# Kernel optimization log

Measured on AMD Instinct MI355X. Metric: run time of the kernel, lower is better.

The kernel has to match this reference:

```python
import jax, jax.numpy as jnp
import numpy as np

N_NODES = 100000
N_EDGES = 1600000
D_IN = 64
D_OUT = 64
BN_EPS = 1e-5


def setup_inputs() -> dict:
    key = jax.random.key(0)
    k1, k2, k3 = jax.random.split(key, 3)
    x = jax.random.normal(k1, (N_NODES, D_IN), dtype=jnp.float32)
    edge_index = jax.random.randint(k2, (2, N_EDGES), 0, N_NODES, dtype=jnp.int64)
    # GCNConv linear weight [out, in], glorot-ish scale
    W = jax.random.normal(k3, (D_OUT, D_IN), dtype=jnp.float32) / np.sqrt(D_IN)
    b = jnp.zeros((D_OUT,), dtype=jnp.float32)
    gamma = jnp.ones((D_OUT,), dtype=jnp.float32)
    beta = jnp.zeros((D_OUT,), dtype=jnp.float32)
    return {"x": x, "edge_index": edge_index, "W": W, "b": b, "gamma": gamma, "beta": beta}


def reference(x, edge_index, W, b, gamma, beta):
    # --- GCNConv: h = x @ W^T, propagate with sym-normalized adjacency + self-loops ---
    h = x @ W.T  # [N, D_OUT]
    src, tgt = edge_index[0], edge_index[1]
    # degree at target nodes, +1 for self-loop
    deg = jax.ops.segment_sum(jnp.ones((src.shape[0],), h.dtype), tgt,
                              num_segments=N_NODES) + 1.0  # [N]
    dinv = jax.lax.rsqrt(deg)
    norm = dinv[src] * dinv[tgt]  # [E]
    # gather -> scale -> scatter-add; self-loop contribution is h / deg
    agg = jax.ops.segment_sum(h[src] * norm[:, None], tgt, num_segments=N_NODES)
    out = agg + h * (1.0 / deg)[:, None] + b  # [N, D_OUT]
    # --- BatchNorm1d (training-mode batch statistics, biased variance) ---
    mean = out.mean(axis=0)
    var = out.var(axis=0)
    y = gamma * (out - mean) * jax.lax.rsqrt(var + BN_EPS) + beta
    # --- ReLU (dropout = identity in eval) ---
    return jax.nn.relu(y)
```

## Files before the change

kernel.cpp:

```cpp
#include <hip/hip_runtime.h>
#include <stdint.h>

#define N_NODES_C 100000
#define N_EDGES_C 1600000
#define DIM 64
#define BN_EPS_C 1e-5f
#define BSH 7
#define NB 782
#define CH 8192

__device__ __forceinline__ int ld_idx(const void* p, int is64, size_t i) {
    if (is64) return (int)((const long long*)p)[i];
    return ((const int*)p)[i];
}

__device__ __forceinline__ float bflo(unsigned int u) {
    return __uint_as_float(u << 16);
}
__device__ __forceinline__ float bfhi(unsigned int u) {
    return __uint_as_float(u & 0xFFFF0000u);
}
__device__ __forceinline__ unsigned short f2bf(float f) {
    unsigned int u = __float_as_uint(f);
    return (unsigned short)((u + 0x7FFF + ((u >> 16) & 1)) >> 16);
}

__global__ void probe_kernel(const unsigned int* __restrict__ p, int* __restrict__ flag) {
    if (threadIdx.x == 0 && blockIdx.x == 0) {
        int is64 = 1;
        for (int i = 1; i < 64; i += 2) {
            if (p[i] != 0u) { is64 = 0; break; }
        }
        *flag = is64;
    }
}

__global__ __launch_bounds__(256) void hist_kernel(const void* __restrict__ ei,
                                                   const int* __restrict__ flag,
                                                   int* __restrict__ bucket_cnt) {
    __shared__ int hist[NB];
    for (int i = threadIdx.x; i < NB; i += 256) hist[i] = 0;
    __syncthreads();
    int is64 = *flag;
    int stride = gridDim.x * blockDim.x;
    for (int e = blockIdx.x * blockDim.x + threadIdx.x; e < N_EDGES_C; e += stride) {
        int tg = ld_idx(ei, is64, (size_t)N_EDGES_C + e);
        atomicAdd(&hist[tg >> BSH], 1);
    }
    __syncthreads();
    for (int i = threadIdx.x; i < NB; i += 256) {
        int c = hist[i];
        if (c) atomicAdd(&bucket_cnt[i], c);
    }
}

__global__ __launch_bounds__(1024) void bucketscan_kernel(const int* __restrict__ bucket_cnt,
                                                          int* __restrict__ bucket_base,
                                                          int* __restrict__ bucket_cursor) {
    __shared__ int s[1024];
    int t = threadIdx.x;
    int v = (t < NB) ? bucket_cnt[t] : 0;
    s[t] = v;
    __syncthreads();
    for (int off = 1; off < 1024; off <<= 1) {
        int u = (t >= off) ? s[t - off] : 0;
        __syncthreads();
        s[t] += u;
        __syncthreads();
    }
    if (t < NB) {
        int excl = s[t] - v;
        bucket_base[t] = excl;
        bucket_cursor[t] = excl;
    }
}

__global__ __launch_bounds__(256) void binscatter_kernel(const void* __restrict__ ei,
                                                         const int* __restrict__ flag,
                                                         int* __restrict__ bucket_cursor,
                                                         unsigned int* __restrict__ csr) {
    __shared__ int hist[NB];
    __shared__ int base[NB];
    int is64 = *flag;
    int e0 = blockIdx.x * CH;
    int eend = min(e0 + CH, N_EDGES_C);
    for (int i = threadIdx.x; i < NB; i += 256) hist[i] = 0;
    __syncthreads();
    for (int e = e0 + threadIdx.x; e < eend; e += 256) {
        int tg = ld_idx(ei, is64, (size_t)N_EDGES_C + e);
        atomicAdd(&hist[tg >> BSH], 1);
    }
    __syncthreads();
    for (int i = threadIdx.x; i < NB; i += 256) {
        int c = hist[i];
        base[i] = c ? atomicAdd(&bucket_cursor[i], c) : 0;
        hist[i] = 0;
    }
    __syncthreads();
    for (int e = e0 + threadIdx.x; e < eend; e += 256) {
        int s  = ld_idx(ei, is64, (size_t)e);
        int tg = ld_idx(ei, is64, (size_t)N_EDGES_C + e);
        int b  = tg >> BSH;
        int tl = tg & 127;
        int pos = base[b] + atomicAdd(&hist[b], 1);
        csr[pos] = ((unsigned int)tl << 17) | (unsigned int)s;
    }
}

__global__ __launch_bounds__(256) void sort_kernel(const unsigned int* __restrict__ csr,
                                                   const int* __restrict__ bucket_base,
                                                   const int* __restrict__ bucket_cnt,
                                                   int* __restrict__ csr2,
                                                   int* __restrict__ rowbase,
                                                   float* __restrict__ dinv,
                                                   float* __restrict__ inv) {
    __shared__ int cnt[128];
    __shared__ int sbase[129];
    __shared__ int cur[128];
    int bk = blockIdx.x;
    int t = threadIdx.x;
    if (t < 128) cnt[t] = 0;
    __syncthreads();
    int base = bucket_base[bk], n = bucket_cnt[bk];
    for (int i = t; i < n; i += 256) {
        atomicAdd(&cnt[csr[base + i] >> 17], 1);
    }
    __syncthreads();
    if (t == 0) {
        int run = 0;
        for (int k = 0; k < 128; ++k) { sbase[k] = run; run += cnt[k]; }
        sbase[128] = run;
    }
    __syncthreads();
    if (t < 128) {
        cur[t] = base + sbase[t];
        int node = (bk << BSH) + t;
        if (node < N_NODES_C) {
            rowbase[node] = base + sbase[t];
            float d = (float)(cnt[t] + 1);
            dinv[node] = rsqrtf(d);
            inv[node]  = 1.0f / d;
        }
    }
    if (bk == 0 && t == 0) rowbase[N_NODES_C] = N_EDGES_C;
    __syncthreads();
    for (int i = t; i < n; i += 256) {
        unsigned int v = csr[base + i];
        int tl = v >> 17;
        int pos = atomicAdd(&cur[tl], 1);
        csr2[pos] = (int)(v & 0x1FFFF);
    }
}

__global__ __launch_bounds__(256) void gemm_kernel(const float* __restrict__ x,
                                                   const float* __restrict__ W,
                                                   unsigned short* __restrict__ hb) {
    __shared__ float Wl[DIM * 65];
    __shared__ float xs[32][DIM];
    int t = threadIdx.x;
    for (int i = t; i < DIM * DIM; i += 256) {
        Wl[(i >> 6) * 65 + (i & 63)] = W[i];
    }
    int r0 = blockIdx.x * 32;
    for (int i = t; i < 32 * DIM; i += 256) {
        int row = i >> 6, col = i & 63;
        int r = r0 + row;
        xs[row][col] = (r < N_NODES_C) ? x[(size_t)r * DIM + col] : 0.0f;
    }
    __syncthreads();
    int wv = t >> 6, c = t & 63;
    for (int it = 0; it < 8; ++it) {
        int rl = it * 4 + wv;
        int r = r0 + rl;
        float acc = 0.0f;
#pragma unroll
        for (int k = 0; k < DIM; ++k) acc += xs[rl][k] * Wl[c * 65 + k];
        if (r < N_NODES_C) hb[(size_t)r * DIM + c] = f2bf(acc);
    }
}

__global__ __launch_bounds__(256) void gather_kernel(const int* __restrict__ csr2,
                                                     const int* __restrict__ rowbase,
                                                     const float* __restrict__ dinv,
                                                     const float* __restrict__ inv,
                                                     const unsigned int* __restrict__ h2,
                                                     const float* __restrict__ b_,
                                                     float2* __restrict__ out,
                                                     float* __restrict__ sums,
                                                     float* __restrict__ sumsq) {
    int lane = threadIdx.x & 63;
    int half = lane >> 5;
    int c2 = lane & 31;
    int wid = blockIdx.x * (blockDim.x >> 6) + (threadIdx.x >> 6);
    int nw = gridDim.x * (blockDim.x >> 6);
    float2 bb = ((const float2*)b_)[c2];
    float s0a = 0.0f, q0a = 0.0f, s1a = 0.0f, q1a = 0.0f;
    for (int p = wid; p < N_NODES_C / 2; p += nw) {
        int t = 2 * p + half;
        int base = rowbase[t];
        int n = rowbase[t + 1] - base;
        float dt = dinv[t];
        float a0 = 0.0f, a1 = 0.0f;
        int j = 0;
        for (; j + 4 <= n; j += 4) {
            int sA = csr2[base + j + 0];
            int sB = csr2[base + j + 1];
            int sC = csr2[base + j + 2];
            int sD = csr2[base + j + 3];
            float wA = dinv[sA] * dt;
            float wB = dinv[sB] * dt;
            float wC = dinv[sC] * dt;
            float wD = dinv[sD] * dt;
            unsigned int uA = h2[(size_t)sA * 32 + c2];
            unsigned int uB = h2[(size_t)sB * 32 + c2];
            unsigned int uC = h2[(size_t)sC * 32 + c2];
            unsigned int uD = h2[(size_t)sD * 32 + c2];
            a0 = fmaf(bflo(uA), wA, a0); a1 = fmaf(bfhi(uA), wA, a1);
            a0 = fmaf(bflo(uB), wB, a0); a1 = fmaf(bfhi(uB), wB, a1);
            a0 = fmaf(bflo(uC), wC, a0); a1 = fmaf(bfhi(uC), wC, a1);
            a0 = fmaf(bflo(uD), wD, a0); a1 = fmaf(bfhi(uD), wD, a1);
        }
        for (; j < n; ++j) {
            int s = csr2[base + j];
            float w = dinv[s] * dt;
            unsigned int u = h2[(size_t)s * 32 + c2];
            a0 = fmaf(bflo(u), w, a0);
            a1 = fmaf(bfhi(u), w, a1);
        }
        unsigned int ut = h2[(size_t)t * 32 + c2];
        float it = inv[t];
        a0 = fmaf(bflo(ut), it, a0) + bb.x;
        a1 = fmaf(bfhi(ut), it, a1) + bb.y;
        out[(size_t)t * 32 + c2] = make_float2(a0, a1);
        s0a += a0; q0a += a0 * a0;
        s1a += a1; q1a += a1 * a1;
    }
    __shared__ float r0[256], r1[256], r2[256], r3[256];
    r0[threadIdx.x] = s0a; r1[threadIdx.x] = q0a;
    r2[threadIdx.x] = s1a; r3[threadIdx.x] = q1a;
    __syncthreads();
    if (threadIdx.x < 32) {
        float S0 = 0, Q0 = 0, S1 = 0, Q1 = 0;
        for (int k = threadIdx.x; k < 256; k += 32) {
            S0 += r0[k]; Q0 += r1[k]; S1 += r2[k]; Q1 += r3[k];
        }
        unsafeAtomicAdd(&sums[2 * threadIdx.x], S0);
        unsafeAtomicAdd(&sums[2 * threadIdx.x + 1], S1);
        unsafeAtomicAdd(&sumsq[2 * threadIdx.x], Q0);
        unsafeAtomicAdd(&sumsq[2 * threadIdx.x + 1], Q1);
    }
}

__global__ void bnparam_kernel(const float* __restrict__ sums,
                               const float* __restrict__ sumsq,
                               const float* __restrict__ gamma,
                               const float* __restrict__ beta,
                               float* __restrict__ scale,
                               float* __restrict__ shift) {
    int c = threadIdx.x;
    if (c < DIM) {
        float m = sums[c] * (1.0f / N_NODES_C);
        float var = sumsq[c] * (1.0f / N_NODES_C) - m * m;
        float sc = gamma[c] * rsqrtf(var + BN_EPS_C);
        scale[c] = sc;
        shift[c] = beta[c] - m * sc;
    }
}

__global__ __launch_bounds__(256) void bnrelu_kernel(float4* __restrict__ out,
                                                     const float* __restrict__ scale,
                                                     const float* __restrict__ shift) {
    const int n4 = N_NODES_C * (DIM / 4);
    int stride = gridDim.x * blockDim.x;
    for (int i = blockIdx.x * blockDim.x + threadIdx.x; i < n4; i += stride) {
        int cb = (i & 15) * 4;
        float4 v = out[i];
        v.x = fmaxf(fmaf(v.x, scale[cb + 0], shift[cb + 0]), 0.0f);
        v.y = fmaxf(fmaf(v.y, scale[cb + 1], shift[cb + 1]), 0.0f);
        v.z = fmaxf(fmaf(v.z, scale[cb + 2], shift[cb + 2]), 0.0f);
        v.w = fmaxf(fmaf(v.w, scale[cb + 3], shift[cb + 3]), 0.0f);
        out[i] = v;
    }
}

extern "C" void kernel_launch(void* const* d_in, const int* in_sizes, int n_in,
                              void* d_out, int out_size, void* d_ws, size_t ws_size,
                              hipStream_t stream) {
    const float* x     = (const float*)d_in[0];
    const void*  ei    = d_in[1];
    const float* W     = (const float*)d_in[2];
    const float* b     = (const float*)d_in[3];
    const float* gamma = (const float*)d_in[4];
    const float* beta  = (const float*)d_in[5];
    float* out = (float*)d_out;

    char* ws = (char*)d_ws;
    int*   flag          = (int*)(ws + 0);
    int*   bucket_cnt    = (int*)(ws + 256);
    int*   bucket_base   = (int*)(ws + 3584);
    int*   bucket_cursor = (int*)(ws + 6912);
    float* dinv          = (float*)(ws + 10240);
    float* inv           = (float*)(ws + 410240);
    int*   rowbase       = (int*)(ws + 810240);
    float* sums          = (float*)(ws + 1210496);
    float* sumsq         = (float*)(ws + 1210752);
    float* scale         = (float*)(ws + 1211008);
    float* shift         = (float*)(ws + 1211264);
    unsigned int* csr    = (unsigned int*)(ws + 1211520);
    int*   csr2          = (int*)(ws + 7611520);
    unsigned short* hb   = (unsigned short*)(ws + 14011520);

    hipMemsetAsync(bucket_cnt, 0, NB * sizeof(int), stream);
    hipMemsetAsync(sums, 0, 512, stream);

    probe_kernel<<<1, 64, 0, stream>>>((const unsigned int*)ei, flag);
    hist_kernel<<<256, 256, 0, stream>>>(ei, flag, bucket_cnt);
    gemm_kernel<<<(N_NODES_C + 31) / 32, 256, 0, stream>>>(x, W, hb);
    bucketscan_kernel<<<1, 1024, 0, stream>>>(bucket_cnt, bucket_base, bucket_cursor);
    binscatter_kernel<<<(N_EDGES_C + CH - 1) / CH, 256, 0, stream>>>(ei, flag,
                                                                    bucket_cursor, csr);
    sort_kernel<<<NB, 256, 0, stream>>>(csr, bucket_base, bucket_cnt, csr2,
                                        rowbase, dinv, inv);
    gather_kernel<<<2048, 256, 0, stream>>>(csr2, rowbase, dinv, inv,
                                            (const unsigned int*)hb, b,
                                            (float2*)out, sums, sumsq);
    bnparam_kernel<<<1, 64, 0, stream>>>(sums, sumsq, gamma, beta, scale, shift);
    bnrelu_kernel<<<1024, 256, 0, stream>>>((float4*)out, scale, shift);
}
```

Baseline: 262.1 us.

## Prescale GEMM output by source dinv to drop per-edge norm gathers

Factors the symmetric normalization so the GEMM writes h*dinv[src] in bf16, and the gather sums raw prescaled rows before multiplying once by dinv[target]. This removes the per-edge dinv[src] random load and the multiply, and removes the inv array because the self-loop term becomes hs[t]*dt. The GEMM now runs after the sort kernel so dinv is available, which removes its overlap freedom. The gather loop is also unrolled to 8 edges. Rounding the prescaled values to bf16 shifts slightly where precision is lost.

```diff
diff --git a/kernel.cpp b/kernel.cpp
--- a/kernel.cpp
+++ b/kernel.cpp
@@ -112,8 +112,7 @@
                                                    const int* __restrict__ bucket_cnt,
                                                    int* __restrict__ csr2,
                                                    int* __restrict__ rowbase,
-                                                   float* __restrict__ dinv,
-                                                   float* __restrict__ inv) {
+                                                   float* __restrict__ dinv) {
     __shared__ int cnt[128];
     __shared__ int sbase[129];
     __shared__ int cur[128];
@@ -139,7 +138,6 @@
             rowbase[node] = base + sbase[t];
             float d = (float)(cnt[t] + 1);
             dinv[node] = rsqrtf(d);
-            inv[node]  = 1.0f / d;
         }
     }
     if (bk == 0 && t == 0) rowbase[N_NODES_C] = N_EDGES_C;
@@ -154,7 +152,8 @@
 
 __global__ __launch_bounds__(256) void gemm_kernel(const float* __restrict__ x,
                                                    const float* __restrict__ W,
-                                                   unsigned short* __restrict__ hb) {
+                                                   const float* __restrict__ dinv,
+                                                   unsigned short* __restrict__ hs) {
     __shared__ float Wl[DIM * 65];
     __shared__ float xs[32][DIM];
     int t = threadIdx.x;
@@ -175,15 +174,14 @@
         float acc = 0.0f;
 #pragma unroll
         for (int k = 0; k < DIM; ++k) acc += xs[rl][k] * Wl[c * 65 + k];
-        if (r < N_NODES_C) hb[(size_t)r * DIM + c] = f2bf(acc);
+        if (r < N_NODES_C) hs[(size_t)r * DIM + c] = f2bf(acc * dinv[r]);
     }
 }
 
 __global__ __launch_bounds__(256) void gather_kernel(const int* __restrict__ csr2,
                                                      const int* __restrict__ rowbase,
                                                      const float* __restrict__ dinv,
-                                                     const float* __restrict__ inv,
-                                                     const unsigned int* __restrict__ h2,
+                                                     const unsigned int* __restrict__ hs2,
                                                      const float* __restrict__ b_,
                                                      float2* __restrict__ out,
                                                      float* __restrict__ sums,
@@ -202,35 +200,48 @@
         float dt = dinv[t];
         float a0 = 0.0f, a1 = 0.0f;
         int j = 0;
-        for (; j + 4 <= n; j += 4) {
+        for (; j + 8 <= n; j += 8) {
             int sA = csr2[base + j + 0];
             int sB = csr2[base + j + 1];
             int sC = csr2[base + j + 2];
             int sD = csr2[base + j + 3];
-            float wA = dinv[sA] * dt;
-            float wB = dinv[sB] * dt;
-            float wC = dinv[sC] * dt;
-            float wD = dinv[sD] * dt;
-            unsigned int uA = h2[(size_t)sA * 32 + c2];
-            unsigned int uB = h2[(size_t)sB * 32 + c2];
-            unsigned int uC = h2[(size_t)sC * 32 + c2];
-            unsigned int uD = h2[(size_t)sD * 32 + c2];
-            a0 = fmaf(bflo(uA), wA, a0); a1 = fmaf(bfhi(uA), wA, a1);
-            a0 = fmaf(bflo(uB), wB, a0); a1 = fmaf(bfhi(uB), wB, a1);
-            a0 = fmaf(bflo(uC), wC, a0); a1 = fmaf(bfhi(uC), wC, a1);
-            a0 = fmaf(bflo(uD), wD, a0); a1 = fmaf(bfhi(uD), wD, a1);
-        }
-        for (; j < n; ++j) {
+            int sE = csr2[base + j + 4];
+            int sF = csr2[base + j + 5];
+            int sG = csr2[base + j + 6];
+            int sH = csr2[base + j + 7];
+            unsigned int uA = hs2[(size_t)sA * 32 + c2];
+            unsigned int uB = hs2[(size_t)sB * 32 + c2];
+            unsigned int uC = hs2[(size_t)sC * 32 + c2];
+            unsigned int uD = hs2[(size_t)sD * 32 + c2];
+            unsigned int uE = hs2[(size_t)sE * 32 + c2];
+            unsigned int uF = hs2[(size_t)sF * 32 + c2];
+            unsigned int uG = hs2[(size_t)sG * 32 + c2];
+            unsigned int uH = hs2[(size_t)sH * 32 + c2];
+            a0 += bflo(uA); a1 += bfhi(uA);
+            a0 += bflo(uB); a1 += bfhi(uB);
+            a0 += bflo(uC); a1 += bfhi(uC);
+            a0 += bflo(uD); a1 += bfhi(uD);
+            a0 += bflo(uE); a1 += bfhi(uE);
+            a0 += bflo(uF); a1 += bfhi(uF);
+            a0 += bflo(uG); a1 += bfhi(uG);
+            a0 += bflo(uH); a1 += bfhi(uH);
+        }
+        for (; j + 2 <= n; j += 2) {
+            int sA = csr2[base + j + 0];
+            int sB = csr2[base + j + 1];
+            unsigned int uA = hs2[(size_t)sA * 32 + c2];
+            unsigned int uB = hs2[(size_t)sB * 32 + c2];
+            a0 += bflo(uA); a1 += bfhi(uA);
+            a0 += bflo(uB); a1 += bfhi(uB);
+        }
+        if (j < n) {
             int s = csr2[base + j];
-            float w = dinv[s] * dt;
-            unsigned int u = h2[(size_t)s * 32 + c2];
-            a0 = fmaf(bflo(u), w, a0);
-            a1 = fmaf(bfhi(u), w, a1);
-        }
-        unsigned int ut = h2[(size_t)t * 32 + c2];
-        float it = inv[t];
-        a0 = fmaf(bflo(ut), it, a0) + bb.x;
-        a1 = fmaf(bfhi(ut), it, a1) + bb.y;
+            unsigned int u = hs2[(size_t)s * 32 + c2];
+            a0 += bflo(u); a1 += bfhi(u);
+        }
+        unsigned int ut = hs2[(size_t)t * 32 + c2];
+        a0 = fmaf(a0 + bflo(ut), dt, bb.x);
+        a1 = fmaf(a1 + bfhi(ut), dt, bb.y);
         out[(size_t)t * 32 + c2] = make_float2(a0, a1);
         s0a += a0; q0a += a0 * a0;
         s1a += a1; q1a += a1 * a1;
@@ -300,29 +311,28 @@
     int*   bucket_base   = (int*)(ws + 3584);
     int*   bucket_cursor = (int*)(ws + 6912);
     float* dinv          = (float*)(ws + 10240);
-    float* inv           = (float*)(ws + 410240);
-    int*   rowbase       = (int*)(ws + 810240);
-    float* sums          = (float*)(ws + 1210496);
-    float* sumsq         = (float*)(ws + 1210752);
-    float* scale         = (float*)(ws + 1211008);
-    float* shift         = (float*)(ws + 1211264);
-    unsigned int* csr    = (unsigned int*)(ws + 1211520);
-    int*   csr2          = (int*)(ws + 7611520);
-    unsigned short* hb   = (unsigned short*)(ws + 14011520);
+    int*   rowbase       = (int*)(ws + 410240);
+    float* sums          = (float*)(ws + 810496);
+    float* sumsq         = (float*)(ws + 810752);
+    float* scale         = (float*)(ws + 811008);
+    float* shift         = (float*)(ws + 811264);
+    unsigned int* csr    = (unsigned int*)(ws + 811520);
+    int*   csr2          = (int*)(ws + 7211520);
+    unsigned short* hs   = (unsigned short*)(ws + 13611520);
 
     hipMemsetAsync(bucket_cnt, 0, NB * sizeof(int), stream);
     hipMemsetAsync(sums, 0, 512, stream);
 
     probe_kernel<<<1, 64, 0, stream>>>((const unsigned int*)ei, flag);
     hist_kernel<<<256, 256, 0, stream>>>(ei, flag, bucket_cnt);
-    gemm_kernel<<<(N_NODES_C + 31) / 32, 256, 0, stream>>>(x, W, hb);
     bucketscan_kernel<<<1, 1024, 0, stream>>>(bucket_cnt, bucket_base, bucket_cursor);
     binscatter_kernel<<<(N_EDGES_C + CH - 1) / CH, 256, 0, stream>>>(ei, flag,
                                                                     bucket_cursor, csr);
     sort_kernel<<<NB, 256, 0, stream>>>(csr, bucket_base, bucket_cnt, csr2,
-                                        rowbase, dinv, inv);
-    gather_kernel<<<2048, 256, 0, stream>>>(csr2, rowbase, dinv, inv,
-                                            (const unsigned int*)hb, b,
+                                        rowbase, dinv);
+    gemm_kernel<<<(N_NODES_C + 31) / 32, 256, 0, stream>>>(x, W, dinv, hs);
+    gather_kernel<<<2048, 256, 0, stream>>>(csr2, rowbase, dinv,
+                                            (const unsigned int*)hs, b,
                                             (float2*)out, sums, sumsq);
     bnparam_kernel<<<1, 64, 0, stream>>>(sums, sumsq, gamma, beta, scale, shift);
     bnrelu_kernel<<<1024, 256, 0, stream>>>((float4*)out, scale, shift);
```

Result: no change. 257.5 us (-1.8%).
